# Optimization experiments

Hardware: AMD Instinct MI355X
Metric: run time of the kernel (lower is better)

The kernel has to match this reference:

```python
import jax, jax.numpy as jnp
import numpy as np

DIM = 1024
HEADS = 8
DIM_HEAD = 64
INNER = HEADS * DIM_HEAD  # 512


def setup_inputs() -> dict:
    key = jax.random.key(0)
    k1, k2, k3, k4 = jax.random.split(key, 4)
    x = jax.random.normal(k1, (4, 4096, DIM), dtype=jnp.float32)
    # torch nn.Linear weights: [out_features, in_features]
    w_qkv = jax.random.normal(k2, (INNER * 3, DIM), dtype=jnp.float32) * (DIM ** -0.5)
    w_out = jax.random.normal(k3, (DIM, INNER), dtype=jnp.float32) * (INNER ** -0.5)
    b_out = jax.random.normal(k4, (DIM,), dtype=jnp.float32) * 0.01
    return {"x": x, "w_qkv": w_qkv, "w_out": w_out, "b_out": b_out}


def reference(x, w_qkv, w_out, b_out):
    b, n, _ = x.shape
    h, dh = HEADS, DIM_HEAD
    qkv = x @ w_qkv.T  # [b, n, 3*inner]
    q, k, v = jnp.split(qkv, 3, axis=-1)
    # [b, n, inner] -> [b, h, n, dh]
    reshape = lambda t: t.reshape(b, n, h, dh).transpose(0, 2, 1, 3)
    q, k, v = reshape(q), reshape(k), reshape(v)
    k = jax.nn.softmax(k, axis=-1)
    context = jnp.einsum('bhnd,bhne->bhde', k, v)   # [b, h, dh, dh]
    out = jnp.einsum('bhnd,bhde->bhne', q, context)  # [b, h, n, dh]
    out = out.transpose(0, 2, 1, 3).reshape(b, n, h * dh)
    return out @ w_out.T + b_out
```

## Files before the change

kernel.cpp:

```cpp
#include <hip/hip_runtime.h>
#include <hip/hip_bf16.h>

using bf16 = __hip_bfloat16;
typedef __attribute__((ext_vector_type(8))) short short8;
typedef __attribute__((ext_vector_type(4))) float floatx4;

#define NB 4
#define NSEQ 4096
#define DIM 1024
#define INNER 512
#define TOK (NB * NSEQ)


__device__ inline unsigned short f2bf(float x) {
  union { bf16 h; unsigned short u; } c; c.h = __float2bfloat16(x); return c.u;
}
__device__ inline float bf2f(unsigned short u) {
  return __uint_as_float((unsigned)u << 16);
}

__device__ inline void gload_lds16(const bf16* g, bf16* ldsbase) {
  __builtin_amdgcn_global_load_lds(
      (const __attribute__((address_space(1))) void*)g,
      (__attribute__((address_space(3))) void*)ldsbase, 16, 0, 0);
}

#define WAITVM(N) asm volatile("s_waitcnt vmcnt(" #N ")" ::: "memory")

__global__ __launch_bounds__(256)
void fused_prep(const float* __restrict__ x, const float* __restrict__ w_qkv,
                bf16* __restrict__ xb, bf16* __restrict__ wkvb,
                bf16* __restrict__ wqT) {
  const int tid = threadIdx.x;
  const int blk = blockIdx.x;

  if (blk < 8192) {
    const size_t i = (size_t)blk * 256 + tid;
    const float* src = x + i * 8;
    const float4 a = ((const float4*)src)[0];
    const float4 b = ((const float4*)src)[1];
    union { uint4 u; bf16 h[8]; } p;
    p.h[0] = __float2bfloat16(a.x); p.h[1] = __float2bfloat16(a.y);
    p.h[2] = __float2bfloat16(a.z); p.h[3] = __float2bfloat16(a.w);
    p.h[4] = __float2bfloat16(b.x); p.h[5] = __float2bfloat16(b.y);
    p.h[6] = __float2bfloat16(b.z); p.h[7] = __float2bfloat16(b.w);
    *(uint4*)(xb + i * 8) = p.u;
  } else if (blk < 8704) {
    const size_t i = (size_t)(blk - 8192) * 256 + tid;
    const float* src = w_qkv + (size_t)INNER * DIM + i * 8;
    const float4 a = ((const float4*)src)[0];
    const float4 b = ((const float4*)src)[1];
    union { uint4 u; bf16 h[8]; } p;
    p.h[0] = __float2bfloat16(a.x); p.h[1] = __float2bfloat16(a.y);
    p.h[2] = __float2bfloat16(a.z); p.h[3] = __float2bfloat16(a.w);
    p.h[4] = __float2bfloat16(b.x); p.h[5] = __float2bfloat16(b.y);
    p.h[6] = __float2bfloat16(b.z); p.h[7] = __float2bfloat16(b.w);
    *(uint4*)(wkvb + i * 8) = p.u;
  } else {
    __shared__ unsigned short t[64 * 68];
    const int q  = blk - 8704;
    const int c0 = (q & 15) * 64;
    const int r0 = (q >> 4) * 64;
#pragma unroll
    for (int l = 0; l < 4; ++l) {
      const int s = l * 256 + tid;
      const int row = s >> 4, col4 = s & 15;
      const float4 v = *(const float4*)(w_qkv + (size_t)(r0 + row) * 1024 + c0 + col4 * 4);
      t[row * 68 + col4 * 4 + 0] = f2bf(v.x);
      t[row * 68 + col4 * 4 + 1] = f2bf(v.y);
      t[row * 68 + col4 * 4 + 2] = f2bf(v.z);
      t[row * 68 + col4 * 4 + 3] = f2bf(v.w);
    }
    __syncthreads();
#pragma unroll
    for (int l = 0; l < 2; ++l) {
      const int s = l * 256 + tid;
      const int cc = s >> 3, g = s & 7;
      union { uint4 u; unsigned short h[8]; } o;
#pragma unroll
      for (int u = 0; u < 8; ++u) o.h[u] = t[(g * 8 + u) * 68 + cc];
      *(uint4*)((unsigned short*)wqT + (size_t)(c0 + cc) * 512 + r0 + g * 8) = o.u;
    }
  }
}

template <typename TO>
__global__ __launch_bounds__(256, 4)
void gemm_bt(const bf16* __restrict__ A, int lda,
             const bf16* __restrict__ W, int mTiles,
             TO* __restrict__ C, int ldc, int K,
             TO* __restrict__ Calt, int msplit) {
  __shared__ __align__(16) bf16 As[128 * 64];
  __shared__ __align__(16) bf16 Bs[128 * 64];

  const int tid    = threadIdx.x;
  const int p      = blockIdx.x;
  const int m_tile = p % mTiles;
  const int n_tile = p / mTiles;
  const int m0     = m_tile * 128;
  const int n0     = n_tile * 128;

  const int wave = tid >> 6;
  const int lane = tid & 63;
  const int wr   = (wave >> 1) * 64;
  const int wc   = (wave & 1) * 64;
  const int quad = lane >> 4;
  const int r16  = lane & 15;
  const int rxor = r16 & 7;
  const int lrow = lane >> 3;
  const int lcol = lane & 7;
  const int gchunk = lcol ^ lrow;

  floatx4 acc[4][4];
#pragma unroll
  for (int i = 0; i < 4; ++i)
#pragma unroll
    for (int j = 0; j < 4; ++j) acc[i][j] = (floatx4)0.0f;

  const int ksteps = K >> 6;
  for (int kt = 0; kt < ksteps; ++kt) {
    const int k0 = kt << 6;
#pragma unroll
    for (int t = 0; t < 4; ++t) {
      const int s   = wave * 4 + t;
      const int row = s * 8 + lrow;
      gload_lds16(A + (size_t)(m0 + row) * lda + k0 + gchunk * 8, As + s * 512);
      gload_lds16(W + (size_t)(n0 + row) * K   + k0 + gchunk * 8, Bs + s * 512);
    }
    __syncthreads();
#pragma unroll
    for (int kk = 0; kk < 64; kk += 32) {
      const int cbase = kk >> 3;
      short8 af[4], bfg[4];
#pragma unroll
      for (int i = 0; i < 4; ++i)
        af[i] = *(const short8*)(As + (wr + i * 16 + r16) * 64 + (((quad + cbase) ^ rxor) << 3));
#pragma unroll
      for (int j = 0; j < 4; ++j)
        bfg[j] = *(const short8*)(Bs + (wc + j * 16 + r16) * 64 + (((quad + cbase) ^ rxor) << 3));
#pragma unroll
      for (int i = 0; i < 4; ++i)
#pragma unroll
        for (int j = 0; j < 4; ++j)
          acc[i][j] = __builtin_amdgcn_mfma_f32_16x16x32_bf16(af[i], bfg[j], acc[i][j], 0, 0, 0);
    }
    __syncthreads();
  }

  TO* Cb = C; int radj = 0;
  if (Calt && m0 >= msplit) { Cb = Calt; radj = msplit; }
#pragma unroll
  for (int j = 0; j < 4; ++j) {
    const int col = n0 + wc + j * 16 + r16;
#pragma unroll
    for (int i = 0; i < 4; ++i) {
      const int rowb = m0 + wr + i * 16 + quad * 4 - radj;
#pragma unroll
      for (int r = 0; r < 4; ++r)
        Cb[(size_t)(rowb + r) * ldc + col] = __float2bfloat16(acc[i][j][r]);
    }
  }
}

__global__ __launch_bounds__(256, 4)
void kv_softmax_ctx(const bf16* __restrict__ A, const bf16* __restrict__ Wkv,
                    float* __restrict__ ctx_part) {
  __shared__ __align__(16) char smem[33280];
  bf16* As = (bf16*)smem;
  bf16* Bs = (bf16*)(smem + 16384);
  unsigned short* skT = (unsigned short*)smem;
  unsigned short* vT  = (unsigned short*)(smem + 16640);

  const int tid    = threadIdx.x;
  const int p      = blockIdx.x;
  const int m_tile = p >> 3;
  const int h      = p & 7;
  const int m0     = m_tile * 128;

  const int wave = tid >> 6;
  const int lane = tid & 63;
  const int wr   = (wave >> 1) * 64;
  const int wc   = (wave & 1) * 64;
  const int quad = lane >> 4;
  const int r16  = lane & 15;
  const int rxor = r16 & 7;
  const int lrow = lane >> 3;
  const int lcol = lane & 7;
  const int gchunk = lcol ^ lrow;

  floatx4 acc[4][4];
#pragma unroll
  for (int i = 0; i < 4; ++i)
#pragma unroll
    for (int j = 0; j < 4; ++j) acc[i][j] = (floatx4)0.0f;

  for (int kt = 0; kt < 16; ++kt) {
    const int k0 = kt << 6;
#pragma unroll
    for (int t = 0; t < 4; ++t) {
      const int s   = wave * 4 + t;
      const int row = s * 8 + lrow;
      const int badd = (s * 8 >= 64) ? (448 + h * 64) : (h * 64);
      gload_lds16(A   + (size_t)(m0 + row) * 1024 + k0 + gchunk * 8, As + s * 512);
      gload_lds16(Wkv + (size_t)(badd + row) * 1024 + k0 + gchunk * 8, Bs + s * 512);
    }
    __syncthreads();
#pragma unroll
    for (int kk = 0; kk < 64; kk += 32) {
      const int cbase = kk >> 3;
      short8 af[4], bfg[4];
#pragma unroll
      for (int i = 0; i < 4; ++i)
        af[i] = *(const short8*)(As + (wr + i * 16 + r16) * 64 + (((quad + cbase) ^ rxor) << 3));
#pragma unroll
      for (int j = 0; j < 4; ++j)
        bfg[j] = *(const short8*)(Bs + (wc + j * 16 + r16) * 64 + (((quad + cbase) ^ rxor) << 3));
#pragma unroll
      for (int i = 0; i < 4; ++i)
#pragma unroll
        for (int j = 0; j < 4; ++j)
          acc[i][j] = __builtin_amdgcn_mfma_f32_16x16x32_bf16(af[i], bfg[j], acc[i][j], 0, 0, 0);
    }
    __syncthreads();
  }

  const int rowbase = wr + quad * 4;
  if ((wave & 1) == 0) {
#pragma unroll
    for (int i = 0; i < 4; ++i)
#pragma unroll
      for (int reg = 0; reg < 4; ++reg) {
        float kf[4];
#pragma unroll
        for (int j = 0; j < 4; ++j) kf[j] = bf2f(f2bf(acc[i][j][reg]));
        float mx = fmaxf(fmaxf(kf[0], kf[1]), fmaxf(kf[2], kf[3]));
        mx = fmaxf(mx, __shfl_xor(mx, 1, 64));
        mx = fmaxf(mx, __shfl_xor(mx, 2, 64));
        mx = fmaxf(mx, __shfl_xor(mx, 4, 64));
        mx = fmaxf(mx, __shfl_xor(mx, 8, 64));
        float e[4]; float s = 0.0f;
#pragma unroll
        for (int j = 0; j < 4; ++j) { e[j] = __expf(kf[j] - mx); s += e[j]; }
        s += __shfl_xor(s, 1, 64);
        s += __shfl_xor(s, 2, 64);
        s += __shfl_xor(s, 4, 64);
        s += __shfl_xor(s, 8, 64);
        const float inv = 1.0f / s;
        const int row = rowbase + i * 16 + reg;
#pragma unroll
        for (int j = 0; j < 4; ++j)
          skT[(j * 16 + r16) * 130 + row] = f2bf(e[j] * inv);
      }
  } else {
#pragma unroll
    for (int i = 0; i < 4; ++i)
#pragma unroll
      for (int reg = 0; reg < 4; ++reg) {
        const int row = rowbase + i * 16 + reg;
#pragma unroll
        for (int j = 0; j < 4; ++j)
          vT[(j * 16 + r16) * 130 + row] = f2bf(acc[i][j][reg]);
      }
  }
  __syncthreads();

  const int d0 = wave * 16;
  floatx4 cacc[4];
#pragma unroll
  for (int j = 0; j < 4; ++j) cacc[j] = (floatx4)0.0f;
#pragma unroll
  for (int kk = 0; kk < 4; ++kk) {
    const int kof = kk * 32 + quad * 8;
    union { short8 v; unsigned u[4]; } afr;
    {
      const unsigned* qa = (const unsigned*)(skT + (d0 + r16) * 130 + kof);
      afr.u[0] = qa[0]; afr.u[1] = qa[1]; afr.u[2] = qa[2]; afr.u[3] = qa[3];
    }
#pragma unroll
    for (int j = 0; j < 4; ++j) {
      union { short8 v; unsigned u[4]; } bfr;
      const unsigned* qb = (const unsigned*)(vT + (j * 16 + r16) * 130 + kof);
      bfr.u[0] = qb[0]; bfr.u[1] = qb[1]; bfr.u[2] = qb[2]; bfr.u[3] = qb[3];
      cacc[j] = __builtin_amdgcn_mfma_f32_16x16x32_bf16(afr.v, bfr.v, cacc[j], 0, 0, 0);
    }
  }

  float* cg = ctx_part + (size_t)(m_tile * 8 + h) * 4096;
#pragma unroll
  for (int j = 0; j < 4; ++j) {
    const int e = j * 16 + r16;
#pragma unroll
    for (int r = 0; r < 4; ++r) {
      const int d = d0 + quad * 4 + r;
      cg[d * 64 + e] = cacc[j][r];
    }
  }
}

template <typename TO, bool BIAS>
__global__ __launch_bounds__(512, 1)
void gemm256f(const float* __restrict__ A,
              const bf16* __restrict__ W, size_t wbatch,
              const bf16* __restrict__ Walt,
              const float* __restrict__ bias,
              TO* __restrict__ C, int ldc, int K) {
  __shared__ __align__(16) bf16 As[2 * 16384];
  __shared__ __align__(16) bf16 Bs[2 * 16384];

  const int tid  = threadIdx.x;
  const int p    = blockIdx.x;
  const int xcd  = p & 7, q = p >> 3;
  const int m_tile = xcd * 8 + (q & 7);
  const int n_tile = q >> 3;
  const int m0 = m_tile * 256, n0 = n_tile * 256;
  const bf16* Wp = W;
  if (wbatch) {
    const int batch = m_tile >> 4;
    Wp = (batch == 3 && Walt) ? Walt : W + (size_t)batch * wbatch;
  }

  const int wave = tid >> 6, lane = tid & 63;
  const int wm = wave >> 2, wn = wave & 3;
  const int quad = lane >> 4, r16 = lane & 15, rxor = r16 & 7;
  const int lrow = lane >> 3, lcol = lane & 7;
  const int gchunk = lcol ^ lrow;
  const int nk = K >> 6;

  const int wr8 = lane >> 3;
  const int c8  = lane & 7;
  const float* Ab = A + (size_t)(m0 + wave * 8 + wr8) * 1024 + c8 * 8;

  auto stageB = [&](int T) {
    bf16* lp = Bs + (T & 1) * 16384;
#pragma unroll
    for (int c = 0; c < 4; ++c) {
      const int rb = c * 64 + wave * 8;
      gload_lds16(Wp + (size_t)(n0 + rb + lrow) * K + T * 64 + gchunk * 8,
                  lp + rb * 64);
    }
  };
  auto loadA = [&](float4* r, int T) {
#pragma unroll
    for (int l = 0; l < 4; ++l) {
      r[2 * l]     = *(const float4*)(Ab + (size_t)l * 65536 + T * 64);
      r[2 * l + 1] = *(const float4*)(Ab + (size_t)l * 65536 + T * 64 + 4);
    }
  };
  auto writeA = [&](const float4* r, int T) {
    bf16* lp = As + (T & 1) * 16384;
#pragma unroll
    for (int l = 0; l < 4; ++l) {
      const int row = l * 64 + wave * 8 + wr8;
      union { uint4 u; unsigned short h[8]; } pk;
      pk.h[0] = f2bf(r[2*l].x);   pk.h[1] = f2bf(r[2*l].y);
      pk.h[2] = f2bf(r[2*l].z);   pk.h[3] = f2bf(r[2*l].w);
      pk.h[4] = f2bf(r[2*l+1].x); pk.h[5] = f2bf(r[2*l+1].y);
      pk.h[6] = f2bf(r[2*l+1].z); pk.h[7] = f2bf(r[2*l+1].w);
      *(uint4*)(lp + row * 64 + ((c8 ^ wr8) << 3)) = pk.u;
    }
  };

  floatx4 acc[8][4];
#pragma unroll
  for (int i = 0; i < 8; ++i)
#pragma unroll
    for (int j = 0; j < 4; ++j) acc[i][j] = (floatx4)0.0f;

  short8 a[4][2], b0[2][2], b1[2][2];

#define LDA_FRAGS(mh) do {                                                    \
  _Pragma("unroll")                                                           \
  for (int i = 0; i < 4; ++i) {                                               \
    const bf16* base = As + db * 16384 +                                      \
        (wm * 128 + (mh) * 64 + i * 16 + r16) * 64;                           \
    a[i][0] = *(const short8*)(base + ((quad ^ rxor) << 3));                  \
    a[i][1] = *(const short8*)(base + (((4 + quad) ^ rxor) << 3));            \
  } } while (0)

#define LDB_FRAGS(bt, nh) do {                                                \
  _Pragma("unroll")                                                           \
  for (int j = 0; j < 2; ++j) {                                               \
    const bf16* base = Bs + db * 16384 +                                      \
        (wn * 64 + (nh) * 32 + j * 16 + r16) * 64;                            \
    bt[j][0] = *(const short8*)(base + ((quad ^ rxor) << 3));                 \
    bt[j][1] = *(const short8*)(base + (((4 + quad) ^ rxor) << 3));           \
  } } while (0)

#define MFMA_QUAD(mh, bt, nh) do {                                            \
  _Pragma("unroll")                                                           \
  for (int i = 0; i < 4; ++i)                                                 \
  _Pragma("unroll")                                                           \
  for (int j = 0; j < 2; ++j) {                                               \
    acc[(mh)*4+i][(nh)*2+j] = __builtin_amdgcn_mfma_f32_16x16x32_bf16(        \
        a[i][0], bt[j][0], acc[(mh)*4+i][(nh)*2+j], 0, 0, 0);                 \
    acc[(mh)*4+i][(nh)*2+j] = __builtin_amdgcn_mfma_f32_16x16x32_bf16(        \
        a[i][1], bt[j][1], acc[(mh)*4+i][(nh)*2+j], 0, 0, 0);                 \
  } } while (0)

  float4 rP[8], rA[8];
  loadA(rP, 0);
  stageB(0);
  if (nk > 1) { loadA(rA, 1); WAITVM(8); }
  else        { WAITVM(0); }
  writeA(rP, 0);
  asm volatile("s_waitcnt lgkmcnt(0)" ::: "memory");
  __builtin_amdgcn_s_barrier();

  for (int T = 0; T < nk; ++T) {
    const int db = T & 1;
    LDA_FRAGS(0); LDB_FRAGS(b0, 0);
    if (T + 1 < nk) stageB(T + 1);
    __builtin_amdgcn_s_barrier();
    __builtin_amdgcn_s_setprio(1);
    MFMA_QUAD(0, b0, 0);
    __builtin_amdgcn_s_setprio(0);
    __builtin_amdgcn_s_barrier();
    LDB_FRAGS(b1, 1);
    __builtin_amdgcn_s_barrier();
    __builtin_amdgcn_s_setprio(1);
    MFMA_QUAD(0, b1, 1);
    __builtin_amdgcn_s_setprio(0);
    if (T + 1 < nk) { WAITVM(4); writeA(rA, T + 1); }
    __builtin_amdgcn_s_barrier();
    LDA_FRAGS(1);
    if (T + 2 < nk) loadA(rA, T + 2);
    __builtin_amdgcn_s_barrier();
    __builtin_amdgcn_s_setprio(1);
    MFMA_QUAD(1, b1, 1);
    MFMA_QUAD(1, b0, 0);
    __builtin_amdgcn_s_setprio(0);
    if (T + 2 < nk) WAITVM(8);
    else            WAITVM(0);
    __builtin_amdgcn_s_barrier();
  }

#undef LDA_FRAGS
#undef LDB_FRAGS
#undef MFMA_QUAD

#pragma unroll
  for (int jj = 0; jj < 4; ++jj) {
    const int col = n0 + wn * 64 + jj * 16 + r16;
    const float bv = BIAS ? bias[col] : 0.0f;
#pragma unroll
    for (int ii = 0; ii < 8; ++ii) {
      const int rowb = m0 + wm * 128 + ii * 16 + quad * 4;
#pragma unroll
      for (int r = 0; r < 4; ++r) {
        const float v = acc[ii][jj][r] + bv;
        if constexpr (sizeof(TO) == 2)
          C[(size_t)(rowb + r) * ldc + col] = __float2bfloat16(v);
        else
          C[(size_t)(rowb + r) * ldc + col] = v;
      }
    }
  }
}

__global__ __launch_bounds__(256)
void build_m2(const float* __restrict__ w_out, const float* __restrict__ ctx_part,
              bf16* __restrict__ M2) {
  __shared__ unsigned short wo_s[128 * 68];
  __shared__ __align__(16) float ctx_s[4096];

  const int tid = threadIdx.x;
  const int bh  = blockIdx.y;
  const int b   = bh >> 3, h = bh & 7;
  const int o0  = blockIdx.x * 128;

#pragma unroll
  for (int l = 0; l < 8; ++l) {
    const int s = l * 256 + tid;
    const int row = s >> 4, col4 = s & 15;
    const float4 v = *(const float4*)(w_out + (size_t)(o0 + row) * 512 + h * 64 + col4 * 4);
    wo_s[row * 68 + col4 * 4 + 0] = f2bf(v.x);
    wo_s[row * 68 + col4 * 4 + 1] = f2bf(v.y);
    wo_s[row * 68 + col4 * 4 + 2] = f2bf(v.z);
    wo_s[row * 68 + col4 * 4 + 3] = f2bf(v.w);
  }
  const float4* cg = (const float4*)(ctx_part + (size_t)(b * 256 + h) * 4096);
#pragma unroll
  for (int l = 0; l < 4; ++l) {
    const int idx = l * 256 + tid;
    float4 s = make_float4(0.f, 0.f, 0.f, 0.f);
#pragma unroll
    for (int sl = 0; sl < 32; ++sl) {
      const float4 v = cg[(size_t)sl * 8192 + idx];
      s.x += v.x; s.y += v.y; s.z += v.z; s.w += v.w;
    }
    ((float4*)ctx_s)[idx] = s;
  }
  __syncthreads();

  const int o_loc = tid & 127;
  const int dbase = (tid >> 7) * 32;
  float acc[32];
#pragma unroll
  for (int d = 0; d < 32; ++d) acc[d] = 0.0f;

  for (int e = 0; e < 64; ++e) {
    const float wf = bf2f(wo_s[o_loc * 68 + e]);
#pragma unroll
    for (int d = 0; d < 32; ++d)
      acc[d] += wf * ctx_s[(dbase + d) * 64 + e];
  }

  union { uint4 u[4]; unsigned short h[32]; } o;
#pragma unroll
  for (int d = 0; d < 32; ++d) o.h[d] = f2bf(acc[d]);
  unsigned short* dst = (unsigned short*)M2 + (size_t)(b * 1024 + o0 + o_loc) * 512 + h * 64 + dbase;
#pragma unroll
  for (int i = 0; i < 4; ++i) ((uint4*)dst)[i] = o.u[i];
}

extern "C" void kernel_launch(void* const* d_in, const int* in_sizes, int n_in,
                              void* d_out, int out_size, void* d_ws, size_t ws_size,
                              hipStream_t stream) {
  const float* x     = (const float*)d_in[0];
  const float* w_qkv = (const float*)d_in[1];
  const float* w_out = (const float*)d_in[2];
  const float* b_out = (const float*)d_in[3];
  float* out = (float*)d_out;

  char* wbuf = (char*)d_in[1];
  char* obuf = (char*)d_out;

  bf16*  xb   = (bf16*)obuf;
  float* ctxp = (float*)(obuf + (size_t)33554432);
  bf16*  wkvb = (bf16*)(obuf + (size_t)50331648);
  bf16*  M2   = (bf16*)(obuf + (size_t)52428800);
  bf16*  wqT  = (bf16*)(obuf + (size_t)56623104);
  bf16*  W2   = (bf16*)wbuf;
  bf16*  W2b3 = (bf16*)d_in[2];

  fused_prep<<<8832, 256, 0, stream>>>(x, w_qkv, xb, wkvb, wqT);

  kv_softmax_ctx<<<1024, 256, 0, stream>>>(xb, wkvb, ctxp);

  build_m2<<<dim3(8, 32), 256, 0, stream>>>(w_out, ctxp, M2);

  gemm_bt<bf16><<<256, 256, 0, stream>>>(
      M2, 512, wqT, 32, W2, 1024, 512, W2b3, 3072);

  gemm256f<float, true><<<256, 512, 0, stream>>>(
      x, W2, (size_t)1048576, W2b3, b_out, out, DIM, DIM);
}
```

Baseline: 265.6 us.

## Fuse fp32-to-bf16 conversion into KV and final GEMMs, drop prep pass

Removes the separate prep kernel that converted x and the KV weights to bf16. The kv_softmax_ctx kernel and a new 128x128-tile final GEMM now load fp32 directly, convert in registers and write to LDS. The wqT transpose is merged into the build_m2 launch. The large pipelined 256x256 final GEMM is replaced by a simpler non-pipelined 128-tile kernel with XCD-aware block mapping. This saves a full write and reread of a bf16 copy of x and two launches, but it reads fp32 x twice, once in each GEMM, and loses the double-buffered pipelining of the old final GEMM.

Measured after the change: 272.0 us. 1.02x slower.

```diff
diff --git a/kernel.cpp b/kernel.cpp
--- a/kernel.cpp
+++ b/kernel.cpp
@@ -18,6 +18,12 @@
 __device__ inline float bf2f(unsigned short u) {
   return __uint_as_float((unsigned)u << 16);
 }
+__device__ inline uint4 pack8(const float4 a, const float4 b) {
+  union { uint4 u; unsigned short h[8]; } p;
+  p.h[0] = f2bf(a.x); p.h[1] = f2bf(a.y); p.h[2] = f2bf(a.z); p.h[3] = f2bf(a.w);
+  p.h[4] = f2bf(b.x); p.h[5] = f2bf(b.y); p.h[6] = f2bf(b.z); p.h[7] = f2bf(b.w);
+  return p.u;
+}
 
 __device__ inline void gload_lds16(const bf16* g, bf16* ldsbase) {
   __builtin_amdgcn_global_load_lds(
@@ -25,47 +31,228 @@
       (__attribute__((address_space(3))) void*)ldsbase, 16, 0, 0);
 }
 
-#define WAITVM(N) asm volatile("s_waitcnt vmcnt(" #N ")" ::: "memory")
+__global__ __launch_bounds__(256, 4)
+void kv_softmax_ctx(const float* __restrict__ x, const float* __restrict__ wq,
+                    float* __restrict__ ctx_part) {
+  __shared__ __align__(16) char smem[33280];
+  bf16* As = (bf16*)smem;
+  bf16* Bs = (bf16*)(smem + 16384);
+  unsigned short* skT = (unsigned short*)smem;
+  unsigned short* vT  = (unsigned short*)(smem + 16640);
+
+  const int tid    = threadIdx.x;
+  const int p      = blockIdx.x;
+  const int h      = (p >> 3) & 7;
+  const int m_tile = (p & 7) + (p >> 6) * 8;
+  const int m0     = m_tile * 128;
+
+  const int wave = tid >> 6;
+  const int lane = tid & 63;
+  const int wr   = (wave >> 1) * 64;
+  const int wc   = (wave & 1) * 64;
+  const int quad = lane >> 4;
+  const int r16  = lane & 15;
+  const int rxor = r16 & 7;
+  const int wr8  = lane >> 3;
+  const int c8   = lane & 7;
+  const int wb   = wave * 8 + wr8;
+
+  const float* Ax = x + (size_t)(m0 + wb) * 1024 + c8 * 8;
+  const float* Bx0 = wq + (size_t)(512 + h * 64 + wb) * 1024 + c8 * 8;
+  const float* Bx2 = wq + (size_t)(960 + h * 64 + 64 + wb) * 1024 + c8 * 8;
+
+  floatx4 acc[4][4];
+#pragma unroll
+  for (int i = 0; i < 4; ++i)
+#pragma unroll
+    for (int j = 0; j < 4; ++j) acc[i][j] = (floatx4)0.0f;
+
+  for (int kt = 0; kt < 16; ++kt) {
+    const int k0 = kt << 6;
+    float4 r[8];
+#pragma unroll
+    for (int l = 0; l < 4; ++l) {
+      r[2 * l]     = *(const float4*)(Ax + (size_t)l * 32768 + k0);
+      r[2 * l + 1] = *(const float4*)(Ax + (size_t)l * 32768 + k0 + 4);
+    }
+#pragma unroll
+    for (int l = 0; l < 4; ++l) {
+      const int row = l * 32 + wb;
+      *(uint4*)(As + row * 64 + ((c8 ^ wr8) << 3)) = pack8(r[2 * l], r[2 * l + 1]);
+    }
+#pragma unroll
+    for (int l = 0; l < 4; ++l) {
+      const float* bp = (l < 2) ? (Bx0 + (size_t)l * 32768)
+                                : (Bx2 + (size_t)(l - 2) * 32768);
+      r[2 * l]     = *(const float4*)(bp + k0);
+      r[2 * l + 1] = *(const float4*)(bp + k0 + 4);
+    }
+#pragma unroll
+    for (int l = 0; l < 4; ++l) {
+      const int row = l * 32 + wb;
+      *(uint4*)(Bs + row * 64 + ((c8 ^ wr8) << 3)) = pack8(r[2 * l], r[2 * l + 1]);
+    }
+    __syncthreads();
+#pragma unroll
+    for (int kk = 0; kk < 64; kk += 32) {
+      const int cbase = kk >> 3;
+      short8 af[4], bfg[4];
+#pragma unroll
+      for (int i = 0; i < 4; ++i)
+        af[i] = *(const short8*)(As + (wr + i * 16 + r16) * 64 + (((quad + cbase) ^ rxor) << 3));
+#pragma unroll
+      for (int j = 0; j < 4; ++j)
+        bfg[j] = *(const short8*)(Bs + (wc + j * 16 + r16) * 64 + (((quad + cbase) ^ rxor) << 3));
+#pragma unroll
+      for (int i = 0; i < 4; ++i)
+#pragma unroll
+        for (int j = 0; j < 4; ++j)
+          acc[i][j] = __builtin_amdgcn_mfma_f32_16x16x32_bf16(af[i], bfg[j], acc[i][j], 0, 0, 0);
+    }
+    __syncthreads();
+  }
+
+  const int rowbase = wr + quad * 4;
+  if ((wave & 1) == 0) {
+#pragma unroll
+    for (int i = 0; i < 4; ++i)
+#pragma unroll
+      for (int reg = 0; reg < 4; ++reg) {
+        float kf[4];
+#pragma unroll
+        for (int j = 0; j < 4; ++j) kf[j] = bf2f(f2bf(acc[i][j][reg]));
+        float mx = fmaxf(fmaxf(kf[0], kf[1]), fmaxf(kf[2], kf[3]));
+        mx = fmaxf(mx, __shfl_xor(mx, 1, 64));
+        mx = fmaxf(mx, __shfl_xor(mx, 2, 64));
+        mx = fmaxf(mx, __shfl_xor(mx, 4, 64));
+        mx = fmaxf(mx, __shfl_xor(mx, 8, 64));
+        float e[4]; float s = 0.0f;
+#pragma unroll
+        for (int j = 0; j < 4; ++j) { e[j] = __expf(kf[j] - mx); s += e[j]; }
+        s += __shfl_xor(s, 1, 64);
+        s += __shfl_xor(s, 2, 64);
+        s += __shfl_xor(s, 4, 64);
+        s += __shfl_xor(s, 8, 64);
+        const float inv = 1.0f / s;
+        const int row = rowbase + i * 16 + reg;
+#pragma unroll
+        for (int j = 0; j < 4; ++j)
+          skT[(j * 16 + r16) * 130 + row] = f2bf(e[j] * inv);
+      }
+  } else {
+#pragma unroll
+    for (int i = 0; i < 4; ++i)
+#pragma unroll
+      for (int reg = 0; reg < 4; ++reg) {
+        const int row = rowbase + i * 16 + reg;
+#pragma unroll
+        for (int j = 0; j < 4; ++j)
+          vT[(j * 16 + r16) * 130 + row] = f2bf(acc[i][j][reg]);
+      }
+  }
+  __syncthreads();
+
+  const int d0 = wave * 16;
+  floatx4 cacc[4];
+#pragma unroll
+  for (int j = 0; j < 4; ++j) cacc[j] = (floatx4)0.0f;
+#pragma unroll
+  for (int kk = 0; kk < 4; ++kk) {
+    const int kof = kk * 32 + quad * 8;
+    union { short8 v; unsigned u[4]; } afr;
+    {
+      const unsigned* qa = (const unsigned*)(skT + (d0 + r16) * 130 + kof);
+      afr.u[0] = qa[0]; afr.u[1] = qa[1]; afr.u[2] = qa[2]; afr.u[3] = qa[3];
+    }
+#pragma unroll
+    for (int j = 0; j < 4; ++j) {
+      union { short8 v; unsigned u[4]; } bfr;
+      const unsigned* qb = (const unsigned*)(vT + (j * 16 + r16) * 130 + kof);
+      bfr.u[0] = qb[0]; bfr.u[1] = qb[1]; bfr.u[2] = qb[2]; bfr.u[3] = qb[3];
+      cacc[j] = __builtin_amdgcn_mfma_f32_16x16x32_bf16(afr.v, bfr.v, cacc[j], 0, 0, 0);
+    }
+  }
+
+  float* cg = ctx_part + (size_t)(m_tile * 8 + h) * 4096;
+#pragma unroll
+  for (int j = 0; j < 4; ++j) {
+    const int e = j * 16 + r16;
+#pragma unroll
+    for (int r = 0; r < 4; ++r) {
+      const int d = d0 + quad * 4 + r;
+      cg[d * 64 + e] = cacc[j][r];
+    }
+  }
+}
 
 __global__ __launch_bounds__(256)
-void fused_prep(const float* __restrict__ x, const float* __restrict__ w_qkv,
-                bf16* __restrict__ xb, bf16* __restrict__ wkvb,
-                bf16* __restrict__ wqT) {
+void build_m2_wqt(const float* __restrict__ w_out, const float* __restrict__ ctx_part,
+                  const float* __restrict__ wq, bf16* __restrict__ M2,
+                  bf16* __restrict__ wqT) {
   const int tid = threadIdx.x;
   const int blk = blockIdx.x;
 
-  if (blk < 8192) {
-    const size_t i = (size_t)blk * 256 + tid;
-    const float* src = x + i * 8;
-    const float4 a = ((const float4*)src)[0];
-    const float4 b = ((const float4*)src)[1];
-    union { uint4 u; bf16 h[8]; } p;
-    p.h[0] = __float2bfloat16(a.x); p.h[1] = __float2bfloat16(a.y);
-    p.h[2] = __float2bfloat16(a.z); p.h[3] = __float2bfloat16(a.w);
-    p.h[4] = __float2bfloat16(b.x); p.h[5] = __float2bfloat16(b.y);
-    p.h[6] = __float2bfloat16(b.z); p.h[7] = __float2bfloat16(b.w);
-    *(uint4*)(xb + i * 8) = p.u;
-  } else if (blk < 8704) {
-    const size_t i = (size_t)(blk - 8192) * 256 + tid;
-    const float* src = w_qkv + (size_t)INNER * DIM + i * 8;
-    const float4 a = ((const float4*)src)[0];
-    const float4 b = ((const float4*)src)[1];
-    union { uint4 u; bf16 h[8]; } p;
-    p.h[0] = __float2bfloat16(a.x); p.h[1] = __float2bfloat16(a.y);
-    p.h[2] = __float2bfloat16(a.z); p.h[3] = __float2bfloat16(a.w);
-    p.h[4] = __float2bfloat16(b.x); p.h[5] = __float2bfloat16(b.y);
-    p.h[6] = __float2bfloat16(b.z); p.h[7] = __float2bfloat16(b.w);
-    *(uint4*)(wkvb + i * 8) = p.u;
+  if (blk < 256) {
+    __shared__ unsigned short wo_s[128 * 68];
+    __shared__ __align__(16) float ctx_s[4096];
+
+    const int bh = blk >> 3;
+    const int b  = bh >> 3, h = bh & 7;
+    const int o0 = (blk & 7) * 128;
+
+#pragma unroll
+    for (int l = 0; l < 8; ++l) {
+      const int s = l * 256 + tid;
+      const int row = s >> 4, col4 = s & 15;
+      const float4 v = *(const float4*)(w_out + (size_t)(o0 + row) * 512 + h * 64 + col4 * 4);
+      wo_s[row * 68 + col4 * 4 + 0] = f2bf(v.x);
+      wo_s[row * 68 + col4 * 4 + 1] = f2bf(v.y);
+      wo_s[row * 68 + col4 * 4 + 2] = f2bf(v.z);
+      wo_s[row * 68 + col4 * 4 + 3] = f2bf(v.w);
+    }
+    const float4* cg = (const float4*)(ctx_part + (size_t)(b * 256 + h) * 4096);
+#pragma unroll
+    for (int l = 0; l < 4; ++l) {
+      const int idx = l * 256 + tid;
+      float4 s = make_float4(0.f, 0.f, 0.f, 0.f);
+#pragma unroll
+      for (int sl = 0; sl < 32; ++sl) {
+        const float4 v = cg[(size_t)sl * 8192 + idx];
+        s.x += v.x; s.y += v.y; s.z += v.z; s.w += v.w;
+      }
+      ((float4*)ctx_s)[idx] = s;
+    }
+    __syncthreads();
+
+    const int o_loc = tid & 127;
+    const int dbase = (tid >> 7) * 32;
+    float acc[32];
+#pragma unroll
+    for (int d = 0; d < 32; ++d) acc[d] = 0.0f;
+
+    for (int e = 0; e < 64; ++e) {
+      const float wf = bf2f(wo_s[o_loc * 68 + e]);
+#pragma unroll
+      for (int d = 0; d < 32; ++d)
+        acc[d] += wf * ctx_s[(dbase + d) * 64 + e];
+    }
+
+    union { uint4 u[4]; unsigned short hh[32]; } o;
+#pragma unroll
+    for (int d = 0; d < 32; ++d) o.hh[d] = f2bf(acc[d]);
+    unsigned short* dst = (unsigned short*)M2 + (size_t)(b * 1024 + o0 + o_loc) * 512 + h * 64 + dbase;
+#pragma unroll
+    for (int i = 0; i < 4; ++i) ((uint4*)dst)[i] = o.u[i];
   } else {
     __shared__ unsigned short t[64 * 68];
-    const int q  = blk - 8704;
+    const int q  = blk - 256;
     const int c0 = (q & 15) * 64;
     const int r0 = (q >> 4) * 64;
 #pragma unroll
     for (int l = 0; l < 4; ++l) {
       const int s = l * 256 + tid;
       const int row = s >> 4, col4 = s & 15;
-      const float4 v = *(const float4*)(w_qkv + (size_t)(r0 + row) * 1024 + c0 + col4 * 4);
+      const float4 v = *(const float4*)(wq + (size_t)(r0 + row) * 1024 + c0 + col4 * 4);
       t[row * 68 + col4 * 4 + 0] = f2bf(v.x);
       t[row * 68 + col4 * 4 + 1] = f2bf(v.y);
       t[row * 68 + col4 * 4 + 2] = f2bf(v.z);
@@ -76,9 +263,9 @@
     for (int l = 0; l < 2; ++l) {
       const int s = l * 256 + tid;
       const int cc = s >> 3, g = s & 7;
-      union { uint4 u; unsigned short h[8]; } o;
-#pragma unroll
-      for (int u = 0; u < 8; ++u) o.h[u] = t[(g * 8 + u) * 68 + cc];
+      union { uint4 u; unsigned short hh[8]; } o;
+#pragma unroll
+      for (int u = 0; u < 8; ++u) o.hh[u] = t[(g * 8 + u) * 68 + cc];
       *(uint4*)((unsigned short*)wqT + (size_t)(c0 + cc) * 512 + r0 + g * 8) = o.u;
     }
   }
@@ -163,19 +350,21 @@
 }
 
 __global__ __launch_bounds__(256, 4)
-void kv_softmax_ctx(const bf16* __restrict__ A, const bf16* __restrict__ Wkv,
-                    float* __restrict__ ctx_part) {
-  __shared__ __align__(16) char smem[33280];
-  bf16* As = (bf16*)smem;
-  bf16* Bs = (bf16*)(smem + 16384);
-  unsigned short* skT = (unsigned short*)smem;
-  unsigned short* vT  = (unsigned short*)(smem + 16640);
+void gemm_f32a(const float* __restrict__ A,
+               const bf16* __restrict__ W, size_t wbatch,
+               const bf16* __restrict__ Walt,
+               const float* __restrict__ bias,
+               float* __restrict__ C, int ldc) {
+  __shared__ __align__(16) bf16 As[128 * 64];
+  __shared__ __align__(16) bf16 Bs[128 * 64];
 
   const int tid    = threadIdx.x;
   const int p      = blockIdx.x;
-  const int m_tile = p >> 3;
-  const int h      = p & 7;
-  const int m0     = m_tile * 128;
+  const int n_tile = (p >> 3) & 7;
+  const int m_tile = (p & 7) + (p >> 6) * 8;
+  const int m0 = m_tile * 128, n0 = n_tile * 128;
+  const int batch = m_tile >> 5;
+  const bf16* Wp = (batch == 3 && Walt) ? Walt : W + (size_t)batch * wbatch;
 
   const int wave = tid >> 6;
   const int lane = tid & 63;
@@ -187,6 +376,9 @@
   const int lrow = lane >> 3;
   const int lcol = lane & 7;
   const int gchunk = lcol ^ lrow;
+  const int wb = wave * 8 + lrow;
+
+  const float* Ax = A + (size_t)(m0 + wb) * 1024 + lcol * 8;
 
   floatx4 acc[4][4];
 #pragma unroll
@@ -196,13 +388,22 @@
 
   for (int kt = 0; kt < 16; ++kt) {
     const int k0 = kt << 6;
+    float4 rA[8];
+#pragma unroll
+    for (int l = 0; l < 4; ++l) {
+      rA[2 * l]     = *(const float4*)(Ax + (size_t)l * 32768 + k0);
+      rA[2 * l + 1] = *(const float4*)(Ax + (size_t)l * 32768 + k0 + 4);
+    }
 #pragma unroll
     for (int t = 0; t < 4; ++t) {
       const int s   = wave * 4 + t;
       const int row = s * 8 + lrow;
-      const int badd = (s * 8 >= 64) ? (448 + h * 64) : (h * 64);
-      gload_lds16(A   + (size_t)(m0 + row) * 1024 + k0 + gchunk * 8, As + s * 512);
-      gload_lds16(Wkv + (size_t)(badd + row) * 1024 + k0 + gchunk * 8, Bs + s * 512);
+      gload_lds16(Wp + (size_t)(n0 + row) * 1024 + k0 + gchunk * 8, Bs + s * 512);
+    }
+#pragma unroll
+    for (int l = 0; l < 4; ++l) {
+      const int row = l * 32 + wb;
+      *(uint4*)(As + row * 64 + ((lcol ^ lrow) << 3)) = pack8(rA[2 * l], rA[2 * l + 1]);
     }
     __syncthreads();
 #pragma unroll
@@ -224,293 +425,18 @@
     __syncthreads();
   }
 
-  const int rowbase = wr + quad * 4;
-  if ((wave & 1) == 0) {
-#pragma unroll
-    for (int i = 0; i < 4; ++i)
-#pragma unroll
-      for (int reg = 0; reg < 4; ++reg) {
-        float kf[4];
-#pragma unroll
-        for (int j = 0; j < 4; ++j) kf[j] = bf2f(f2bf(acc[i][j][reg]));
-        float mx = fmaxf(fmaxf(kf[0], kf[1]), fmaxf(kf[2], kf[3]));
-        mx = fmaxf(mx, __shfl_xor(mx, 1, 64));
-        mx = fmaxf(mx, __shfl_xor(mx, 2, 64));
-        mx = fmaxf(mx, __shfl_xor(mx, 4, 64));
-        mx = fmaxf(mx, __shfl_xor(mx, 8, 64));
-        float e[4]; float s = 0.0f;
-#pragma unroll
-        for (int j = 0; j < 4; ++j) { e[j] = __expf(kf[j] - mx); s += e[j]; }
-        s += __shfl_xor(s, 1, 64);
-        s += __shfl_xor(s, 2, 64);
-        s += __shfl_xor(s, 4, 64);
-        s += __shfl_xor(s, 8, 64);
-        const float inv = 1.0f / s;
-        const int row = rowbase + i * 16 + reg;
-#pragma unroll
-        for (int j = 0; j < 4; ++j)
-          skT[(j * 16 + r16) * 130 + row] = f2bf(e[j] * inv);
-      }
-  } else {
-#pragma unroll
-    for (int i = 0; i < 4; ++i)
-#pragma unroll
-      for (int reg = 0; reg < 4; ++reg) {
-        const int row = rowbase + i * 16 + reg;
-#pragma unroll
-        for (int j = 0; j < 4; ++j)
-          vT[(j * 16 + r16) * 130 + row] = f2bf(acc[i][j][reg]);
-      }
-  }
-  __syncthreads();
-
-  const int d0 = wave * 16;
-  floatx4 cacc[4];
-#pragma unroll
-  for (int j = 0; j < 4; ++j) cacc[j] = (floatx4)0.0f;
-#pragma unroll
-  for (int kk = 0; kk < 4; ++kk) {
-    const int kof = kk * 32 + quad * 8;
-    union { short8 v; unsigned u[4]; } afr;
-    {
-      const unsigned* qa = (const unsigned*)(skT + (d0 + r16) * 130 + kof);
-      afr.u[0] = qa[0]; afr.u[1] = qa[1]; afr.u[2] = qa[2]; afr.u[3] = qa[3];
-    }
-#pragma unroll
-    for (int j = 0; j < 4; ++j) {
-      union { short8 v; unsigned u[4]; } bfr;
-      const unsigned* qb = (const unsigned*)(vT + (j * 16 + r16) * 130 + kof);
-      bfr.u[0] = qb[0]; bfr.u[1] = qb[1]; bfr.u[2] = qb[2]; bfr.u[3] = qb[3];
-      cacc[j] = __builtin_amdgcn_mfma_f32_16x16x32_bf16(afr.v, bfr.v, cacc[j], 0, 0, 0);
-    }
-  }
-
-  float* cg = ctx_part + (size_t)(m_tile * 8 + h) * 4096;
 #pragma unroll
   for (int j = 0; j < 4; ++j) {
-    const int e = j * 16 + r16;
-#pragma unroll
-    for (int r = 0; r < 4; ++r) {
-      const int d = d0 + quad * 4 + r;
-      cg[d * 64 + e] = cacc[j][r];
-    }
-  }
-}
-
-template <typename TO, bool BIAS>
-__global__ __launch_bounds__(512, 1)
-void gemm256f(const float* __restrict__ A,
-              const bf16* __restrict__ W, size_t wbatch,
-              const bf16* __restrict__ Walt,
-              const float* __restrict__ bias,
-              TO* __restrict__ C, int ldc, int K) {
-  __shared__ __align__(16) bf16 As[2 * 16384];
-  __shared__ __align__(16) bf16 Bs[2 * 16384];
-
-  const int tid  = threadIdx.x;
-  const int p    = blockIdx.x;
-  const int xcd  = p & 7, q = p >> 3;
-  const int m_tile = xcd * 8 + (q & 7);
-  const int n_tile = q >> 3;
-  const int m0 = m_tile * 256, n0 = n_tile * 256;
-  const bf16* Wp = W;
-  if (wbatch) {
-    const int batch = m_tile >> 4;
-    Wp = (batch == 3 && Walt) ? Walt : W + (size_t)batch * wbatch;
-  }
-
-  const int wave = tid >> 6, lane = tid & 63;
-  const int wm = wave >> 2, wn = wave & 3;
-  const int quad = lane >> 4, r16 = lane & 15, rxor = r16 & 7;
-  const int lrow = lane >> 3, lcol = lane & 7;
-  const int gchunk = lcol ^ lrow;
-  const int nk = K >> 6;
-
-  const int wr8 = lane >> 3;
-  const int c8  = lane & 7;
-  const float* Ab = A + (size_t)(m0 + wave * 8 + wr8) * 1024 + c8 * 8;
-
-  auto stageB = [&](int T) {
-    bf16* lp = Bs + (T & 1) * 16384;
-#pragma unroll
-    for (int c = 0; c < 4; ++c) {
-      const int rb = c * 64 + wave * 8;
-      gload_lds16(Wp + (size_t)(n0 + rb + lrow) * K + T * 64 + gchunk * 8,
-                  lp + rb * 64);
-    }
-  };
-  auto loadA = [&](float4* r, int T) {
-#pragma unroll
-    for (int l = 0; l < 4; ++l) {
-      r[2 * l]     = *(const float4*)(Ab + (size_t)l * 65536 + T * 64);
-      r[2 * l + 1] = *(const float4*)(Ab + (size_t)l * 65536 + T * 64 + 4);
-    }
-  };
-  auto writeA = [&](const float4* r, int T) {
-    bf16* lp = As + (T & 1) * 16384;
-#pragma unroll
-    for (int l = 0; l < 4; ++l) {
-      const int row = l * 64 + wave * 8 + wr8;
-      union { uint4 u; unsigned short h[8]; } pk;
-      pk.h[0] = f2bf(r[2*l].x);   pk.h[1] = f2bf(r[2*l].y);
-      pk.h[2] = f2bf(r[2*l].z);   pk.h[3] = f2bf(r[2*l].w);
-      pk.h[4] = f2bf(r[2*l+1].x); pk.h[5] = f2bf(r[2*l+1].y);
-      pk.h[6] = f2bf(r[2*l+1].z); pk.h[7] = f2bf(r[2*l+1].w);
-      *(uint4*)(lp + row * 64 + ((c8 ^ wr8) << 3)) = pk.u;
-    }
-  };
-
-  floatx4 acc[8][4];
-#pragma unroll
-  for (int i = 0; i < 8; ++i)
-#pragma unroll
-    for (int j = 0; j < 4; ++j) acc[i][j] = (floatx4)0.0f;
-
-  short8 a[4][2], b0[2][2], b1[2][2];
-
-#define LDA_FRAGS(mh) do {                                                    \
-  _Pragma("unroll")                                                           \
-  for (int i = 0; i < 4; ++i) {                                               \
-    const bf16* base = As + db * 16384 +                                      \
-        (wm * 128 + (mh) * 64 + i * 16 + r16) * 64;                           \
-    a[i][0] = *(const short8*)(base + ((quad ^ rxor) << 3));                  \
-    a[i][1] = *(const short8*)(base + (((4 + quad) ^ rxor) << 3));            \
-  } } while (0)
-
-#define LDB_FRAGS(bt, nh) do {                                                \
-  _Pragma("unroll")                                                           \
-  for (int j = 0; j < 2; ++j) {                                               \
-    const bf16* base = Bs + db * 16384 +                                      \
-        (wn * 64 + (nh) * 32 + j * 16 + r16) * 64;                            \
-    bt[j][0] = *(const short8*)(base + ((quad ^ rxor) << 3));                 \
-    bt[j][1] = *(const short8*)(base + (((4 + quad) ^ rxor) << 3));           \
-  } } while (0)
-
-#define MFMA_QUAD(mh, bt, nh) do {                                            \
-  _Pragma("unroll")                                                           \
-  for (int i = 0; i < 4; ++i)                                                 \
-  _Pragma("unroll")                                                           \
-  for (int j = 0; j < 2; ++j) {                                               \
-    acc[(mh)*4+i][(nh)*2+j] = __builtin_amdgcn_mfma_f32_16x16x32_bf16(        \
-        a[i][0], bt[j][0], acc[(mh)*4+i][(nh)*2+j], 0, 0, 0);                 \
-    acc[(mh)*4+i][(nh)*2+j] = __builtin_amdgcn_mfma_f32_16x16x32_bf16(        \
-        a[i][1], bt[j][1], acc[(mh)*4+i][(nh)*2+j], 0, 0, 0);                 \
-  } } while (0)
-
-  float4 rP[8], rA[8];
-  loadA(rP, 0);
-  stageB(0);
-  if (nk > 1) { loadA(rA, 1); WAITVM(8); }
-  else        { WAITVM(0); }
-  writeA(rP, 0);
-  asm volatile("s_waitcnt lgkmcnt(0)" ::: "memory");
-  __builtin_amdgcn_s_barrier();
-
-  for (int T = 0; T < nk; ++T) {
-    const int db = T & 1;
-    LDA_FRAGS(0); LDB_FRAGS(b0, 0);
-    if (T + 1 < nk) stageB(T + 1);
-    __builtin_amdgcn_s_barrier();
-    __builtin_amdgcn_s_setprio(1);
-    MFMA_QUAD(0, b0, 0);
-    __builtin_amdgcn_s_setprio(0);
-    __builtin_amdgcn_s_barrier();
-    LDB_FRAGS(b1, 1);
-    __builtin_amdgcn_s_barrier();
-    __builtin_amdgcn_s_setprio(1);
-    MFMA_QUAD(0, b1, 1);
-    __builtin_amdgcn_s_setprio(0);
-    if (T + 1 < nk) { WAITVM(4); writeA(rA, T + 1); }
-    __builtin_amdgcn_s_barrier();
-    LDA_FRAGS(1);
-    if (T + 2 < nk) loadA(rA, T + 2);
-    __builtin_amdgcn_s_barrier();
-    __builtin_amdgcn_s_setprio(1);
-    MFMA_QUAD(1, b1, 1);
-    MFMA_QUAD(1, b0, 0);
-    __builtin_amdgcn_s_setprio(0);
-    if (T + 2 < nk) WAITVM(8);
-    else            WAITVM(0);
-    __builtin_amdgcn_s_barrier();
-  }
-
-#undef LDA_FRAGS
-#undef LDB_FRAGS
-#undef MFMA_QUAD
-
-#pragma unroll
-  for (int jj = 0; jj < 4; ++jj) {
-    const int col = n0 + wn * 64 + jj * 16 + r16;
-    const float bv = BIAS ? bias[col] : 0.0f;
-#pragma unroll
-    for (int ii = 0; ii < 8; ++ii) {
-      const int rowb = m0 + wm * 128 + ii * 16 + quad * 4;
-#pragma unroll
-      for (int r = 0; r < 4; ++r) {
-        const float v = acc[ii][jj][r] + bv;
-        if constexpr (sizeof(TO) == 2)
-          C[(size_t)(rowb + r) * ldc + col] = __float2bfloat16(v);
-        else
-          C[(size_t)(rowb + r) * ldc + col] = v;
-      }
-    }
-  }
-}
-
-__global__ __launch_bounds__(256)
-void build_m2(const float* __restrict__ w_out, const float* __restrict__ ctx_part,
-              bf16* __restrict__ M2) {
-  __shared__ unsigned short wo_s[128 * 68];
-  __shared__ __align__(16) float ctx_s[4096];
-
-  const int tid = threadIdx.x;
-  const int bh  = blockIdx.y;
-  const int b   = bh >> 3, h = bh & 7;
-  const int o0  = blockIdx.x * 128;
-
-#pragma unroll
-  for (int l = 0; l < 8; ++l) {
-    const int s = l * 256 + tid;
-    const int row = s >> 4, col4 = s & 15;
-    const float4 v = *(const float4*)(w_out + (size_t)(o0 + row) * 512 + h * 64 + col4 * 4);
-    wo_s[row * 68 + col4 * 4 + 0] = f2bf(v.x);
-    wo_s[row * 68 + col4 * 4 + 1] = f2bf(v.y);
-    wo_s[row * 68 + col4 * 4 + 2] = f2bf(v.z);
-    wo_s[row * 68 + col4 * 4 + 3] = f2bf(v.w);
-  }
-  const float4* cg = (const float4*)(ctx_part + (size_t)(b * 256 + h) * 4096);
-#pragma unroll
-  for (int l = 0; l < 4; ++l) {
-    const int idx = l * 256 + tid;
-    float4 s = make_float4(0.f, 0.f, 0.f, 0.f);
-#pragma unroll
-    for (int sl = 0; sl < 32; ++sl) {
-      const float4 v = cg[(size_t)sl * 8192 + idx];
-      s.x += v.x; s.y += v.y; s.z += v.z; s.w += v.w;
-    }
-    ((float4*)ctx_s)[idx] = s;
-  }
-  __syncthreads();
-
-  const int o_loc = tid & 127;
-  const int dbase = (tid >> 7) * 32;
-  float acc[32];
-#pragma unroll
-  for (int d = 0; d < 32; ++d) acc[d] = 0.0f;
-
-  for (int e = 0; e < 64; ++e) {
-    const float wf = bf2f(wo_s[o_loc * 68 + e]);
-#pragma unroll
-    for (int d = 0; d < 32; ++d)
-      acc[d] += wf * ctx_s[(dbase + d) * 64 + e];
-  }
-
-  union { uint4 u[4]; unsigned short h[32]; } o;
-#pragma unroll
-  for (int d = 0; d < 32; ++d) o.h[d] = f2bf(acc[d]);
-  unsigned short* dst = (unsigned short*)M2 + (size_t)(b * 1024 + o0 + o_loc) * 512 + h * 64 + dbase;
-#pragma unroll
-  for (int i = 0; i < 4; ++i) ((uint4*)dst)[i] = o.u[i];
+    const int col = n0 + wc + j * 16 + r16;
+    const float bv = bias[col];
+#pragma unroll
+    for (int i = 0; i < 4; ++i) {
+      const int rowb = m0 + wr + i * 16 + quad * 4;
+#pragma unroll
+      for (int r = 0; r < 4; ++r)
+        C[(size_t)(rowb + r) * ldc + col] = acc[i][j][r] + bv;
+    }
+  }
 }
 
 extern "C" void kernel_launch(void* const* d_in, const int* in_sizes, int n_in,
@@ -525,23 +451,19 @@
   char* wbuf = (char*)d_in[1];
   char* obuf = (char*)d_out;
 
-  bf16*  xb   = (bf16*)obuf;
-  float* ctxp = (float*)(obuf + (size_t)33554432);
-  bf16*  wkvb = (bf16*)(obuf + (size_t)50331648);
-  bf16*  M2   = (bf16*)(obuf + (size_t)52428800);
-  bf16*  wqT  = (bf16*)(obuf + (size_t)56623104);
+  float* ctxp = (float*)obuf;
+  bf16*  M2   = (bf16*)(obuf + (size_t)16777216);
+  bf16*  wqT  = (bf16*)(obuf + (size_t)20971520);
   bf16*  W2   = (bf16*)wbuf;
   bf16*  W2b3 = (bf16*)d_in[2];
 
-  fused_prep<<<8832, 256, 0, stream>>>(x, w_qkv, xb, wkvb, wqT);
-
-  kv_softmax_ctx<<<1024, 256, 0, stream>>>(xb, wkvb, ctxp);
-
-  build_m2<<<dim3(8, 32), 256, 0, stream>>>(w_out, ctxp, M2);
+  kv_softmax_ctx<<<1024, 256, 0, stream>>>(x, w_qkv, ctxp);
+
+  build_m2_wqt<<<384, 256, 0, stream>>>(w_out, ctxp, w_qkv, M2, wqT);
 
   gemm_bt<bf16><<<256, 256, 0, stream>>>(
       M2, 512, wqT, 32, W2, 1024, 512, W2b3, 3072);
 
-  gemm256f<float, true><<<256, 512, 0, stream>>>(
-      x, W2, (size_t)1048576, W2b3, b_out, out, DIM, DIM);
-}
+  gemm_f32a<<<1024, 256, 0, stream>>>(
+      x, W2, (size_t)1048576, W2b3, b_out, out, DIM);
+}
```
